# Kernel tuning notes

Measured on AMD Instinct MI355X. Metric: run time of the kernel, lower is better.

The kernel has to match this reference:

```python
import jax, jax.numpy as jnp
import numpy as np

EPS = 1e-8  # torch cosine_similarity eps
B, N, M = 8192, 128, 64


def setup_inputs() -> dict:
    key = jax.random.key(0)
    ks = jax.random.split(key, 9)
    memory = jax.random.normal(ks[0], (B, N, M), dtype=jnp.float32) * 0.1
    prev_w = jax.random.uniform(ks[1], (B, N), dtype=jnp.float32)
    prev_w = prev_w / prev_w.sum(axis=1, keepdims=True)  # valid attention weighting
    k = jax.random.normal(ks[2], (B, M), dtype=jnp.float32)
    beta = jax.random.uniform(ks[3], (B, 1), dtype=jnp.float32) * 5.0  # key strength > 0
    g = jax.random.uniform(ks[4], (B, 1), dtype=jnp.float32)           # gate in [0,1)
    s = jax.nn.softmax(jax.random.normal(ks[5], (3,), dtype=jnp.float32))  # shift kernel
    y = 1.0 + jax.random.uniform(ks[6], (B, 1), dtype=jnp.float32) * 2.0   # sharpen >= 1
    e = jax.random.uniform(ks[7], (B, M), dtype=jnp.float32)           # erase in [0,1)
    a = jax.random.normal(ks[8], (B, M), dtype=jnp.float32)            # add vector
    return {"memory": memory, "prev_w": prev_w, "k": k, "beta": beta,
            "g": g, "s": s, "y": y, "e": e, "a": a}


def reference(memory, prev_w, k, beta, g, s, y, e, a):
    # --- content addressing: cosine similarity + softmax(beta * sim) ---
    dot = jnp.einsum('bm,bnm->bn', k, memory)                       # (B,N)
    k_norm = jnp.maximum(jnp.linalg.norm(k, axis=-1, keepdims=True), EPS)  # (B,1)
    m_norm = jnp.maximum(jnp.linalg.norm(memory, axis=-1), EPS)     # (B,N)
    cos = dot / (k_norm * m_norm)
    wc = jax.nn.softmax(beta * cos, axis=1)
    # --- interpolation with previous weighting ---
    wg = g * wc + (1.0 - g) * prev_w
    # --- circular convolution shift (cross-correlation with len-3 kernel, pad=1) ---
    # wt[b,i] = s[0]*wg[b,i-1] + s[1]*wg[b,i] + s[2]*wg[b,i+1]  (indices mod N)
    wt = s[0] * jnp.roll(wg, 1, axis=1) + s[1] * wg + s[2] * jnp.roll(wg, -1, axis=1)
    # --- sharpen: power then renormalize ---
    wp = wt ** y
    w = wp / wp.sum(axis=1, keepdims=True)
    # --- read from (old) memory ---
    read = jnp.einsum('bn,bnm->bm', w, memory)
    # --- erase/add write via batched outer products ---
    mem_new = memory * (1.0 - w[:, :, None] * e[:, None, :]) + w[:, :, None] * a[:, None, :]
    return read, mem_new, w
```

## Files before the change

kernel.cpp:

```cpp
#include <hip/hip_runtime.h>
#include <math.h>

constexpr int Bn = 8192;
constexpr int Nn = 128;
constexpr int Mn = 64;
constexpr float kEPS = 1e-8f;

constexpr int ROWP4 = 17;

__global__ __launch_bounds__(256)
void ntm_step(const float* __restrict__ memory,
              const float* __restrict__ prev_w,
              const float* __restrict__ kvec,
              const float* __restrict__ beta,
              const float* __restrict__ gate,
              const float* __restrict__ shift,
              const float* __restrict__ gamma,
              const float* __restrict__ erase,
              const float* __restrict__ addv,
              float* __restrict__ out_read,
              float* __restrict__ out_mem,
              float* __restrict__ out_w)
{
  __shared__ float lm[Nn * ROWP4 * 4];
  __shared__ float lk[Mn];
  __shared__ float le[Mn];
  __shared__ float la[Mn];
  __shared__ float llog[Nn];
  __shared__ float lwg[Nn];
  __shared__ float lw[Nn];
  __shared__ float lpart[16 * Mn];

  const int b = blockIdx.x;
  const int t = threadIdx.x;

  const float4* gm4 = (const float4*)(memory + (size_t)b * (Nn * Mn));

  if (t < Mn) {
    lk[t] = kvec[b * Mn + t];
    le[t] = erase[b * Mn + t];
    la[t] = addv[b * Mn + t];
  }

  float4 stg[8];
  #pragma unroll
  for (int i = 0; i < 8; ++i) stg[i] = gm4[t + 256 * i];
  #pragma unroll
  for (int i = 0; i < 8; ++i) {
    const int f = t + 256 * i;
    ((float4*)lm)[(f >> 4) * ROWP4 + (f & 15)] = stg[i];
  }
  __syncthreads();

  {
    const int n = t >> 1;
    const int half = t & 1;
    const float4* r4 = ((const float4*)lm) + n * ROWP4 + half * 8;
    const float4* k4 = ((const float4*)lk) + half * 8;
    float dot = 0.f, sq = 0.f, ksq = 0.f;
    #pragma unroll
    for (int j = 0; j < 8; ++j) {
      const float4 v = r4[j];
      const float4 kk = k4[j];
      dot += v.x * kk.x + v.y * kk.y + v.z * kk.z + v.w * kk.w;
      sq  += v.x * v.x + v.y * v.y + v.z * v.z + v.w * v.w;
      ksq += kk.x * kk.x + kk.y * kk.y + kk.z * kk.z + kk.w * kk.w;
    }
    dot += __shfl_xor(dot, 1);
    sq  += __shfl_xor(sq, 1);
    ksq += __shfl_xor(ksq, 1);
    if (half == 0) {
      const float kn = fmaxf(sqrtf(ksq), kEPS);
      const float mn = fmaxf(sqrtf(sq), kEPS);
      llog[n] = beta[b] * (dot / (kn * mn));
    }
  }
  __syncthreads();

  if (t < 64) {
    const float v0 = llog[t], v1 = llog[t + 64];
    float mx = fmaxf(v0, v1);
    #pragma unroll
    for (int o = 1; o < 64; o <<= 1) mx = fmaxf(mx, __shfl_xor(mx, o));
    const float e0 = __expf(v0 - mx), e1 = __expf(v1 - mx);
    float sum = e0 + e1;
    #pragma unroll
    for (int o = 1; o < 64; o <<= 1) sum += __shfl_xor(sum, o);
    const float inv = 1.f / sum;
    const float gv = gate[b];
    lwg[t]      = gv * (e0 * inv) + (1.f - gv) * prev_w[b * Nn + t];
    lwg[t + 64] = gv * (e1 * inv) + (1.f - gv) * prev_w[b * Nn + t + 64];
  }
  __syncthreads();

  if (t < 64) {
    const float s0 = shift[0], s1 = shift[1], s2 = shift[2];
    const int n0 = t, n1 = t + 64;
    const float wt0 = s0 * lwg[(n0 - 1) & 127] + s1 * lwg[n0] + s2 * lwg[(n0 + 1) & 127];
    const float wt1 = s0 * lwg[(n1 - 1) & 127] + s1 * lwg[n1] + s2 * lwg[(n1 + 1) & 127];
    const float yv = gamma[b];
    const float wp0 = powf(wt0, yv);
    const float wp1 = powf(wt1, yv);
    float sum = wp0 + wp1;
    #pragma unroll
    for (int o = 1; o < 64; o <<= 1) sum += __shfl_xor(sum, o);
    const float inv = 1.f / sum;
    const float w0 = wp0 * inv, w1 = wp1 * inv;
    lw[n0] = w0;
    lw[n1] = w1;
    out_w[b * Nn + n0] = w0;
    out_w[b * Nn + n1] = w1;
  }
  __syncthreads();

  {
    const int c4 = t & 15;
    const int rbase = t >> 4;
    const float4 ev = ((const float4*)le)[c4];
    const float4 av = ((const float4*)la)[c4];
    float4* om4 = (float4*)(out_mem + (size_t)b * (Nn * Mn));
    float4 racc = make_float4(0.f, 0.f, 0.f, 0.f);
    #pragma unroll
    for (int i = 0; i < 8; ++i) {
      const int row = rbase + 16 * i;
      const float wv = lw[row];
      const float4 mv = ((const float4*)lm)[row * ROWP4 + c4];
      float4 o;
      o.x = mv.x * (1.f - wv * ev.x) + wv * av.x;
      o.y = mv.y * (1.f - wv * ev.y) + wv * av.y;
      o.z = mv.z * (1.f - wv * ev.z) + wv * av.z;
      o.w = mv.w * (1.f - wv * ev.w) + wv * av.w;
      om4[t + 256 * i] = o;
      racc.x += wv * mv.x;
      racc.y += wv * mv.y;
      racc.z += wv * mv.z;
      racc.w += wv * mv.w;
    }
    ((float4*)lpart)[rbase * 16 + c4] = racc;
  }
  __syncthreads();

  if (t < Mn) {
    float acc = 0.f;
    #pragma unroll
    for (int p = 0; p < 16; ++p) acc += lpart[p * Mn + t];
    out_read[b * Mn + t] = acc;
  }
}

extern "C" void kernel_launch(void* const* d_in, const int* in_sizes, int n_in,
                              void* d_out, int out_size, void* d_ws, size_t ws_size,
                              hipStream_t stream) {
  const float* memory = (const float*)d_in[0];
  const float* prev_w = (const float*)d_in[1];
  const float* k      = (const float*)d_in[2];
  const float* beta   = (const float*)d_in[3];
  const float* g      = (const float*)d_in[4];
  const float* s      = (const float*)d_in[5];
  const float* y      = (const float*)d_in[6];
  const float* e      = (const float*)d_in[7];
  const float* a      = (const float*)d_in[8];

  float* out = (float*)d_out;
  float* out_read = out;
  float* out_mem  = out + (size_t)Bn * Mn;
  float* out_w    = out + (size_t)Bn * Mn + (size_t)Bn * Nn * Mn;

  ntm_step<<<Bn, 256, 0, stream>>>(memory, prev_w, k, beta, g, s, y, e, a,
                                   out_read, out_mem, out_w);
}
```

Baseline: 456.6 us.

## Keep memory tile in registers and stage only per-chunk dot/norm partials in LDS

Each thread now keeps its eight float4 memory chunks in registers for the whole kernel instead of copying the full 128x64 tile into shared memory. It computes per-chunk dot and squared-norm partials and writes only those float2 pairs to LDS for the row reductions. The key norm is computed with a 16-lane shuffle, and the key, erase and add vectors are read straight from global memory into registers. This cuts LDS footprint and traffic, which could allow more blocks per CU, in exchange for higher register pressure from holding the tile across the barriers.

```diff
diff --git a/kernel.cpp b/kernel.cpp
--- a/kernel.cpp
+++ b/kernel.cpp
@@ -6,7 +6,7 @@
 constexpr int Mn = 64;
 constexpr float kEPS = 1e-8f;
 
-constexpr int ROWP4 = 17;
+constexpr int DSP = 17;
 
 __global__ __launch_bounds__(256)
 void ntm_step(const float* __restrict__ memory,
@@ -22,10 +22,7 @@
               float* __restrict__ out_mem,
               float* __restrict__ out_w)
 {
-  __shared__ float lm[Nn * ROWP4 * 4];
-  __shared__ float lk[Mn];
-  __shared__ float le[Mn];
-  __shared__ float la[Mn];
+  __shared__ float2 ds2[Nn * DSP];
   __shared__ float llog[Nn];
   __shared__ float lwg[Nn];
   __shared__ float lw[Nn];
@@ -33,42 +30,41 @@
 
   const int b = blockIdx.x;
   const int t = threadIdx.x;
+  const int c4 = t & 15;
+  const int g  = t >> 4;
 
   const float4* gm4 = (const float4*)(memory + (size_t)b * (Nn * Mn));
-
-  if (t < Mn) {
-    lk[t] = kvec[b * Mn + t];
-    le[t] = erase[b * Mn + t];
-    la[t] = addv[b * Mn + t];
-  }
 
   float4 stg[8];
   #pragma unroll
   for (int i = 0; i < 8; ++i) stg[i] = gm4[t + 256 * i];
+
+  const float4 kf = ((const float4*)(kvec  + b * Mn))[c4];
+  const float4 ef = ((const float4*)(erase + b * Mn))[c4];
+  const float4 af = ((const float4*)(addv  + b * Mn))[c4];
+
+  float ksq = kf.x * kf.x + kf.y * kf.y + kf.z * kf.z + kf.w * kf.w;
+  #pragma unroll
+  for (int o = 1; o < 16; o <<= 1) ksq += __shfl_xor(ksq, o);
+
   #pragma unroll
   for (int i = 0; i < 8; ++i) {
-    const int f = t + 256 * i;
-    ((float4*)lm)[(f >> 4) * ROWP4 + (f & 15)] = stg[i];
+    const float4 v = stg[i];
+    float d = v.x * kf.x + v.y * kf.y + v.z * kf.z + v.w * kf.w;
+    float q = v.x * v.x + v.y * v.y + v.z * v.z + v.w * v.w;
+    ds2[(g + 16 * i) * DSP + c4] = make_float2(d, q);
   }
   __syncthreads();
 
   {
     const int n = t >> 1;
     const int half = t & 1;
-    const float4* r4 = ((const float4*)lm) + n * ROWP4 + half * 8;
-    const float4* k4 = ((const float4*)lk) + half * 8;
-    float dot = 0.f, sq = 0.f, ksq = 0.f;
+    const float2* p = ds2 + n * DSP + half * 8;
+    float dot = 0.f, sq = 0.f;
     #pragma unroll
-    for (int j = 0; j < 8; ++j) {
-      const float4 v = r4[j];
-      const float4 kk = k4[j];
-      dot += v.x * kk.x + v.y * kk.y + v.z * kk.z + v.w * kk.w;
-      sq  += v.x * v.x + v.y * v.y + v.z * v.z + v.w * v.w;
-      ksq += kk.x * kk.x + kk.y * kk.y + kk.z * kk.z + kk.w * kk.w;
-    }
+    for (int j = 0; j < 8; ++j) { dot += p[j].x; sq += p[j].y; }
     dot += __shfl_xor(dot, 1);
     sq  += __shfl_xor(sq, 1);
-    ksq += __shfl_xor(ksq, 1);
     if (half == 0) {
       const float kn = fmaxf(sqrtf(ksq), kEPS);
       const float mn = fmaxf(sqrtf(sq), kEPS);
@@ -114,29 +110,24 @@
   __syncthreads();
 
   {
-    const int c4 = t & 15;
-    const int rbase = t >> 4;
-    const float4 ev = ((const float4*)le)[c4];
-    const float4 av = ((const float4*)la)[c4];
     float4* om4 = (float4*)(out_mem + (size_t)b * (Nn * Mn));
     float4 racc = make_float4(0.f, 0.f, 0.f, 0.f);
     #pragma unroll
     for (int i = 0; i < 8; ++i) {
-      const int row = rbase + 16 * i;
-      const float wv = lw[row];
-      const float4 mv = ((const float4*)lm)[row * ROWP4 + c4];
+      const float wv = lw[g + 16 * i];
+      const float4 mv = stg[i];
       float4 o;
-      o.x = mv.x * (1.f - wv * ev.x) + wv * av.x;
-      o.y = mv.y * (1.f - wv * ev.y) + wv * av.y;
-      o.z = mv.z * (1.f - wv * ev.z) + wv * av.z;
-      o.w = mv.w * (1.f - wv * ev.w) + wv * av.w;
+      o.x = mv.x * (1.f - wv * ef.x) + wv * af.x;
+      o.y = mv.y * (1.f - wv * ef.y) + wv * af.y;
+      o.z = mv.z * (1.f - wv * ef.z) + wv * af.z;
+      o.w = mv.w * (1.f - wv * ef.w) + wv * af.w;
       om4[t + 256 * i] = o;
       racc.x += wv * mv.x;
       racc.y += wv * mv.y;
       racc.z += wv * mv.z;
       racc.w += wv * mv.w;
     }
-    ((float4*)lpart)[rbase * 16 + c4] = racc;
+    ((float4*)lpart)[g * 16 + c4] = racc;
   }
   __syncthreads();
 
```

Result: no change. 459.9 us (+0.7%).
